# Kernel tuning notes

Measured on AMD Instinct MI355X. Metric: run time of the kernel, lower is better.

Reference implementation:

```python
import jax, jax.numpy as jnp
import numpy as np
import math


def setup_inputs() -> dict:
    key = jax.random.key(0)
    k1, k2, k3 = jax.random.split(key, 3)
    img = jax.random.normal(k1, (32, 3, 512, 512), dtype=jnp.float32)
    c_u = jax.random.normal(k2, (100, 100), dtype=jnp.float32)  # scalar-field mode coeffs for dx
    c_v = jax.random.normal(k3, (100, 100), dtype=jnp.float32)  # scalar-field mode coeffs for dy
    return {"img": img, "c_u": c_u, "c_v": c_v}


def _scalar_field(c, n):
    # random scalar field of size n x n from the first m modes (m = c.shape[0])
    m = c.shape[0]
    x = jnp.linspace(0.0, 1.0, n, dtype=c.dtype)            # [n]
    k = jnp.arange(1, m + 1, dtype=c.dtype)                 # [m]
    i, j = jnp.meshgrid(k, k, indexing='ij')                # [m, m]
    r = jnp.sqrt(i ** 2 + j ** 2)
    e = (r < m + 0.5).astype(c.dtype) / r                   # sqrt(1/energy) per mode
    s = jnp.sin(jnp.pi * x[:, None] * k[None, :])           # [n, m]
    return jnp.einsum('ij,xi,yj->yx', c * e, s, s)          # [n, n]


def reference(img, c_u, c_v):
    n = img.shape[-1]  # square image assumed (n x n)
    m = c_u.shape[0]   # frequency cutoff `cut`

    # temperature_range(n, cut), deterministic T = midpoint of allowed range (alpha=1)
    log_cut = math.log(m + 1e-06)
    T1 = 1.0 / (math.pi * n ** 2 * log_cut)
    T2 = 4.0 / (math.pi ** 3 * m ** 2 * log_cut)
    T2 = max(T1, T2)
    T = 0.5 * (T1 + T2)

    # displacement fields [n, n]
    dx = (T ** 0.5) * _scalar_field(c_u, n) * n
    dy = (T ** 0.5) * _scalar_field(c_v, n) * n

    # remap with bilinear ('linear') interpolation
    dtype = dx.dtype
    y, x = jnp.meshgrid(jnp.arange(n, dtype=dtype), jnp.arange(n, dtype=dtype), indexing='ij')
    xn = jnp.clip(x - dx, 0.0, n - 1)
    yn = jnp.clip(y - dy, 0.0, n - 1)

    xf = jnp.floor(xn).astype(jnp.int32)
    yf = jnp.floor(yn).astype(jnp.int32)
    xc = jnp.ceil(xn).astype(jnp.int32)
    yc = jnp.ceil(yn).astype(jnp.int32)
    xv = xn - xf.astype(dtype)
    yv = yn - yf.astype(dtype)

    out = ((1 - yv) * (1 - xv) * img[..., yf, xf]
           + (1 - yv) * xv * img[..., yf, xc]
           + yv * (1 - xv) * img[..., yc, xf]
           + yv * xv * img[..., yc, xc])
    return out
```

## Files before the change

### kernel.cpp

```cpp
#include <hip/hip_runtime.h>
#include <math.h>

#define NN 512
#define MM 100
#define TPB 256
#define ROWS_OUT 8
#define ROWS_LDS 24
#define PLANES_PER_BLOCK 8
#define PXPT 16

typedef float f32x4 __attribute__((ext_vector_type(4)));


__global__ void sin_table_kernel(float* __restrict__ St) {
    int tid = blockIdx.x * blockDim.x + threadIdx.x;
    if (tid >= NN * MM) return;
    int x = tid / MM, j = tid % MM;
    double arg = M_PI * ((double)x / (double)(NN - 1)) * (double)(j + 1);
    St[tid] = (float)sin(arg);
}

__global__ void bcoef_kernel(const float* __restrict__ St,
                             const float* __restrict__ c_u,
                             const float* __restrict__ c_v,
                             float* __restrict__ B_u,
                             float* __restrict__ B_v) {
    int x = blockIdx.x;
    int j = threadIdx.x;
    if (j >= MM) return;
    float au = 0.f, av = 0.f;
    for (int i = 0; i < MM; ++i) {
        int i1 = i + 1, j1 = j + 1;
        int r2i = i1 * i1 + j1 * j1;
        float w = (r2i <= 10100) ? (1.0f / sqrtf((float)r2i)) : 0.0f;
        float sw = St[x * MM + i] * w;
        au += sw * c_u[i * MM + j];
        av += sw * c_v[i * MM + j];
    }
    B_u[j * NN + x] = au;
    B_v[j * NN + x] = av;
}

__global__ void field_kernel(const float* __restrict__ St,
                             const float* __restrict__ B_u,
                             const float* __restrict__ B_v,
                             float scale,
                             float* __restrict__ dx,
                             float* __restrict__ dy) {
    int tid = blockIdx.x * blockDim.x + threadIdx.x;
    if (tid >= NN * NN) return;
    int y = tid / NN, x = tid % NN;
    float du = 0.f, dv = 0.f;
    #pragma unroll 4
    for (int j = 0; j < MM; ++j) {
        float s = St[y * MM + j];
        du += B_u[j * NN + x] * s;
        dv += B_v[j * NN + x] * s;
    }
    dx[tid] = scale * du;
    dy[tid] = scale * dv;
}

__global__ __launch_bounds__(TPB, 3)
void remap_kernel(const float* __restrict__ img,
                  const float* __restrict__ dx,
                  const float* __restrict__ dy,
                  float* __restrict__ out,
                  int planes) {
    __shared__ __align__(16) float rows[ROWS_LDS * NN + 2];
    __shared__ int s_mn[4], s_mx[4];
    __shared__ int s_r0, s_nr;

    int nb = gridDim.x;
    int bid = blockIdx.x;
    int sid = (bid & 7) * (nb >> 3) + (bid >> 3);
    int strip = sid & 63;
    int pg    = sid >> 6;

    int t = threadIdx.x;
    int Y = strip * ROWS_OUT;

    float w00[PXPT], w01[PXPT], w10[PXPT], w11[PXPT];
    int offA[PXPT], offB[PXPT];
    int myf = NN, Myc = -1;
    #pragma unroll
    for (int i = 0; i < PXPT; ++i) {
        int xi = ((i & 1) << 8) + t;
        int yi = Y + (i >> 1);
        int pix = (yi << 9) + xi;
        float xn = fminf(fmaxf((float)xi - dx[pix], 0.0f), (float)(NN - 1));
        float yn = fminf(fmaxf((float)yi - dy[pix], 0.0f), (float)(NN - 1));
        int xf = (int)floorf(xn), yf = (int)floorf(yn);
        int yc = (int)ceilf(yn);
        float xv = xn - (float)xf, yv = yn - (float)yf;
        w00[i] = (1.f - yv) * (1.f - xv);
        w01[i] = (1.f - yv) * xv;
        w10[i] = yv * (1.f - xv);
        w11[i] = yv * xv;
        offA[i] = (yf << 9) + xf;
        offB[i] = (yc << 9) + xf;
        myf = min(myf, yf);
        Myc = max(Myc, yc);
    }

    for (int d = 32; d; d >>= 1) {
        myf = min(myf, __shfl_xor(myf, d));
        Myc = max(Myc, __shfl_xor(Myc, d));
    }
    int wid = t >> 6;
    if ((t & 63) == 0) { s_mn[wid] = myf; s_mx[wid] = Myc; }
    if (t < 2) rows[ROWS_LDS * NN + t] = 0.f;
    __syncthreads();
    if (t == 0) {
        int a = min(min(s_mn[0], s_mn[1]), min(s_mn[2], s_mn[3]));
        int b = max(max(s_mx[0], s_mx[1]), max(s_mx[2], s_mx[3]));
        s_r0 = a; s_nr = b - a + 1;
    }
    __syncthreads();
    int r0 = s_r0, nr = s_nr;

    int p0 = pg * PLANES_PER_BLOCK;
    int p1 = p0 + PLANES_PER_BLOCK; if (p1 > planes) p1 = planes;

    if (nr <= ROWS_LDS) {
        int rb = r0 << 9;
        #pragma unroll
        for (int i = 0; i < PXPT; ++i) { offA[i] -= rb; offB[i] -= rb; }

        int nbytes = nr << 11;
        for (int p = p0; p < p1; ++p) {
            const char* ip = (const char*)(img + (size_t)p * (NN * NN) + rb);
            for (int off = t * 16; off < nbytes; off += TPB * 16) {
                *(f32x4*)((char*)rows + off) = *(const f32x4*)(ip + off);
            }
            __syncthreads();
            float* op = out + (size_t)p * (NN * NN);
            #pragma unroll
            for (int i = 0; i < PXPT; ++i) {
                float a0 = rows[offA[i]];
                float a1 = rows[offA[i] + 1];
                float b0 = rows[offB[i]];
                float b1 = rows[offB[i] + 1];
                float o = w00[i] * a0 + w01[i] * a1 + w10[i] * b0 + w11[i] * b1;
                int xi = ((i & 1) << 8) + t;
                int yi = Y + (i >> 1);
                __builtin_nontemporal_store(o, op + (yi << 9) + xi);
            }
            __syncthreads();
        }
    } else {
        for (int p = p0; p < p1; ++p) {
            const float* __restrict__ ip = img + (size_t)p * (NN * NN);
            float* op = out + (size_t)p * (NN * NN);
            #pragma unroll
            for (int i = 0; i < PXPT; ++i) {
                int e1 = ((offA[i] & 511) == 511) ? 0 : 1;
                float a0 = ip[offA[i]], a1 = ip[offA[i] + e1];
                float b0 = ip[offB[i]], b1 = ip[offB[i] + e1];
                float o = w00[i] * a0 + w01[i] * a1 + w10[i] * b0 + w11[i] * b1;
                int xi = ((i & 1) << 8) + t;
                int yi = Y + (i >> 1);
                __builtin_nontemporal_store(o, op + (yi << 9) + xi);
            }
        }
    }
}

extern "C" void kernel_launch(void* const* d_in, const int* in_sizes, int n_in,
                              void* d_out, int out_size, void* d_ws, size_t ws_size,
                              hipStream_t stream) {
    const float* img = (const float*)d_in[0];
    const float* c_u = (const float*)d_in[1];
    const float* c_v = (const float*)d_in[2];
    float* out = (float*)d_out;

    int planes = in_sizes[0] / (NN * NN);

    float* ws  = (float*)d_ws;
    float* St  = ws;
    float* B_u = St  + NN * MM;
    float* B_v = B_u + MM * NN;
    float* dx  = B_v + MM * NN;
    float* dy  = dx  + NN * NN;

    double log_cut = log((double)MM + 1e-6);
    double T1 = 1.0 / (M_PI * (double)NN * (double)NN * log_cut);
    double T2 = 4.0 / (M_PI * M_PI * M_PI * (double)MM * (double)MM * log_cut);
    if (T2 < T1) T2 = T1;
    double T = 0.5 * (T1 + T2);
    float scale = (float)(sqrt(T) * (double)NN);

    sin_table_kernel<<<(NN * MM + 255) / 256, 256, 0, stream>>>(St);
    bcoef_kernel<<<NN, 128, 0, stream>>>(St, c_u, c_v, B_u, B_v);
    field_kernel<<<(NN * NN + 255) / 256, 256, 0, stream>>>(St, B_u, B_v, scale, dx, dy);

    int strips = NN / ROWS_OUT;
    int groups = (planes + PLANES_PER_BLOCK - 1) / PLANES_PER_BLOCK;
    remap_kernel<<<strips * groups, TPB, 0, stream>>>(img, dx, dy, out, planes);
}
```

Before: 85.66 us.

## Register-tile field kernel over rows and shrink remap LDS for higher occupancy

The field kernel now has each thread compute 4 rows by 2 columns, staging the sine rows in shared memory so every B_u/B_v load is reused across rows. This removes most redundant global loads of the coefficient matrices. Separately, the remap kernel's LDS row buffer drops from 24 to 18 rows and launch bounds target 4 blocks per CU, to raise occupancy. In exchange, strips whose displacement spans more than 18 rows fall back to the slower direct-global path. The padding zero is now written just past the rows actually used.

```diff
diff --git a/kernel.cpp b/kernel.cpp
--- a/kernel.cpp
+++ b/kernel.cpp
@@ -5,7 +5,7 @@
 #define MM 100
 #define TPB 256
 #define ROWS_OUT 8
-#define ROWS_LDS 24
+#define ROWS_LDS 18
 #define PLANES_PER_BLOCK 8
 #define PXPT 16
 
@@ -41,33 +41,52 @@
     B_v[j * NN + x] = av;
 }
 
-__global__ void field_kernel(const float* __restrict__ St,
-                             const float* __restrict__ B_u,
-                             const float* __restrict__ B_v,
-                             float scale,
-                             float* __restrict__ dx,
-                             float* __restrict__ dy) {
-    int tid = blockIdx.x * blockDim.x + threadIdx.x;
-    if (tid >= NN * NN) return;
-    int y = tid / NN, x = tid % NN;
-    float du = 0.f, dv = 0.f;
-    #pragma unroll 4
+#define ROWS_F 4
+__global__ __launch_bounds__(256)
+void field_kernel(const float* __restrict__ St,
+                  const float* __restrict__ B_u,
+                  const float* __restrict__ B_v,
+                  float scale,
+                  float* __restrict__ dx,
+                  float* __restrict__ dy) {
+    __shared__ float sS[ROWS_F * MM];
+    int t = threadIdx.x;
+    int y0 = blockIdx.x * ROWS_F;
+
+    for (int i = t; i < ROWS_F * MM; i += 256) {
+        int r = i / MM, j = i % MM;
+        sS[i] = St[(y0 + r) * MM + j];
+    }
+    __syncthreads();
+
+    float au[ROWS_F][2] = {}, av[ROWS_F][2] = {};
     for (int j = 0; j < MM; ++j) {
-        float s = St[y * MM + j];
-        du += B_u[j * NN + x] * s;
-        dv += B_v[j * NN + x] * s;
-    }
-    dx[tid] = scale * du;
-    dy[tid] = scale * dv;
-}
-
-__global__ __launch_bounds__(TPB, 3)
+        float bu0 = B_u[j * NN + t], bu1 = B_u[j * NN + t + 256];
+        float bv0 = B_v[j * NN + t], bv1 = B_v[j * NN + t + 256];
+        #pragma unroll
+        for (int r = 0; r < ROWS_F; ++r) {
+            float s = sS[r * MM + j];
+            au[r][0] += bu0 * s; au[r][1] += bu1 * s;
+            av[r][0] += bv0 * s; av[r][1] += bv1 * s;
+        }
+    }
+    #pragma unroll
+    for (int r = 0; r < ROWS_F; ++r) {
+        int row = (y0 + r) * NN;
+        dx[row + t]       = scale * au[r][0];
+        dx[row + t + 256] = scale * au[r][1];
+        dy[row + t]       = scale * av[r][0];
+        dy[row + t + 256] = scale * av[r][1];
+    }
+}
+
+__global__ __launch_bounds__(TPB, 4)
 void remap_kernel(const float* __restrict__ img,
                   const float* __restrict__ dx,
                   const float* __restrict__ dy,
                   float* __restrict__ out,
                   int planes) {
-    __shared__ __align__(16) float rows[ROWS_LDS * NN + 2];
+    __shared__ __align__(16) float rows[ROWS_LDS * NN + 1];
     __shared__ int s_mn[4], s_mx[4];
     __shared__ int s_r0, s_nr;
 
@@ -109,12 +128,12 @@
     }
     int wid = t >> 6;
     if ((t & 63) == 0) { s_mn[wid] = myf; s_mx[wid] = Myc; }
-    if (t < 2) rows[ROWS_LDS * NN + t] = 0.f;
     __syncthreads();
     if (t == 0) {
         int a = min(min(s_mn[0], s_mn[1]), min(s_mn[2], s_mn[3]));
         int b = max(max(s_mx[0], s_mx[1]), max(s_mx[2], s_mx[3]));
         s_r0 = a; s_nr = b - a + 1;
+        rows[(b - a + 1) * NN] = 0.f;
     }
     __syncthreads();
     int r0 = s_r0, nr = s_nr;
@@ -192,7 +211,7 @@
 
     sin_table_kernel<<<(NN * MM + 255) / 256, 256, 0, stream>>>(St);
     bcoef_kernel<<<NN, 128, 0, stream>>>(St, c_u, c_v, B_u, B_v);
-    field_kernel<<<(NN * NN + 255) / 256, 256, 0, stream>>>(St, B_u, B_v, scale, dx, dy);
+    field_kernel<<<NN / ROWS_F, 256, 0, stream>>>(St, B_u, B_v, scale, dx, dy);
 
     int strips = NN / ROWS_OUT;
     int groups = (planes + PLANES_PER_BLOCK - 1) / PLANES_PER_BLOCK;
```

New measurement: 174.6 us. 104% more time.
